# Kernel optimization log

Measured on AMD Instinct MI355X. Metric: run time of the kernel, lower is better.

The kernel has to match this reference:

```python
import jax, jax.numpy as jnp
import numpy as np

N = 50000      # nodes
E = 800000     # edges
NF = 128       # node_features
BF = 16        # bond_features
H = 4          # heads
C = 32         # hidden_size (per-head out channels)
HC = H * C     # 128 == NF, so all GAT layers share weight shape
DEPTH = 5
NEG_SLOPE = 0.2


def _sanitize(t):
    return jnp.nan_to_num(t, nan=0.0, posinf=1000.0, neginf=-1000.0)


def setup_inputs() -> dict:
    key = jax.random.key(0)
    ks = jax.random.split(key, 12)
    s = 0.1
    x = jax.random.normal(ks[0], (N, NF), jnp.float32)
    edge_index = jax.random.randint(ks[1], (2, E), 0, N, dtype=jnp.int32)
    edge_attr = jax.random.uniform(ks[2], (E, BF), jnp.float32)
    W = jax.random.normal(ks[3], (DEPTH, NF, HC), jnp.float32) * s
    att_src = jax.random.normal(ks[4], (DEPTH, H, C), jnp.float32) * s
    att_dst = jax.random.normal(ks[5], (DEPTH, H, C), jnp.float32) * s
    We = jax.random.normal(ks[6], (DEPTH, BF, HC), jnp.float32) * s
    att_edge = jax.random.normal(ks[7], (DEPTH, H, C), jnp.float32) * s
    b = jnp.zeros((DEPTH, HC), jnp.float32)
    Wout = jax.random.normal(ks[8], (NF + HC, C), jnp.float32) * s
    bout = jnp.zeros((C,), jnp.float32)
    return {"x": x, "edge_index": edge_index, "edge_attr": edge_attr,
            "W": W, "att_src": att_src, "att_dst": att_dst,
            "We": We, "att_edge": att_edge, "b": b,
            "Wout": Wout, "bout": bout}


def _gat_layer(h, s2, d2, ea, W_l, as_l, ad_l, We_l, ae_l, b_l):
    # h: [N, in_dim]; s2/d2: [E+N] edges incl. self loops; ea: [E+N, BF]
    xp = (h @ W_l).reshape(N, H, C)                     # lin(x), view per-head
    a_s = jnp.sum(xp * as_l, axis=-1)                   # [N, H]
    a_d = jnp.sum(xp * ad_l, axis=-1)                   # [N, H]
    ee = (ea @ We_l).reshape(-1, H, C)                  # lin_edge(edge_attr)
    a_e = jnp.sum(ee * ae_l, axis=-1)                   # [E+N, H]
    alpha = jax.nn.leaky_relu(a_s[s2] + a_d[d2] + a_e, NEG_SLOPE)
    # segment softmax over edges grouped by destination node
    m = jax.ops.segment_max(alpha, d2, num_segments=N)  # every node has a self loop -> finite
    ex = jnp.exp(alpha - m[d2])
    den = jax.ops.segment_sum(ex, d2, num_segments=N)
    coef = ex / (den[d2] + 1e-16)                       # [E+N, H]
    out = jax.ops.segment_sum(coef[:, :, None] * xp[s2], d2, num_segments=N)
    return out.reshape(N, HC) + b_l


def reference(x, edge_index, edge_attr, W, att_src, att_dst, We, att_edge, b, Wout, bout):
    src, dst = edge_index[0], edge_index[1]
    # add self loops with fill_value='mean': self-loop attr = mean of incoming edge_attr
    deg = jax.ops.segment_sum(jnp.ones((E,), edge_attr.dtype), dst, num_segments=N)
    sl_attr = jax.ops.segment_sum(edge_attr, dst, num_segments=N) / jnp.maximum(deg, 1.0)[:, None]
    ea = jnp.concatenate([edge_attr, sl_attr], axis=0)          # [E+N, BF]
    loop = jnp.arange(N, dtype=src.dtype)
    s2 = jnp.concatenate([src, loop])
    d2 = jnp.concatenate([dst, loop])

    h = _sanitize(x)
    for l in range(DEPTH):
        h = _gat_layer(h, s2, d2, ea, W[l], att_src[l], att_dst[l], We[l], att_edge[l], b[l])
        h = jax.nn.relu(h)            # dropout is a no-op in eval mode
        h = _sanitize(h)
    h_cat = jnp.concatenate([x, h], axis=1)             # [N, NF+HC]
    out = jax.nn.relu(h_cat @ Wout + bout)
    return _sanitize(out)
```

## Files before the change

kernel.cpp:

```cpp
#include <hip/hip_runtime.h>

#define NN 50000
#define NE 800000
#define NF 128
#define BF 16
#define NH 4
#define HC 128
#define CC 32
#define DEPTH 5
#define NEG 0.2f

typedef __attribute__((ext_vector_type(8))) short bf16x8;
typedef __attribute__((ext_vector_type(4))) float f32x4;

__device__ inline unsigned short f2bf(float f) {
  union { float f; unsigned u; } v; v.f = f;
  unsigned r = v.u + 0x7fff + ((v.u >> 16) & 1);
  return (unsigned short)(r >> 16);
}
__device__ inline float bf2f(unsigned short u) {
  union { unsigned u; float f; } v; v.u = (unsigned)u << 16; return v.f;
}

__global__ void k_count(const int* __restrict__ dst, int* __restrict__ deg) {
  int e = blockIdx.x * 256 + threadIdx.x;
  if (e < NE) atomicAdd(&deg[dst[e]], 1);
}

__global__ void k_partial(const int* __restrict__ deg, int* __restrict__ bsum) {
  __shared__ int s[256];
  int t = threadIdx.x;
  int i = blockIdx.x * 256 + t;
  s[t] = (i < NN) ? deg[i] : 0;
  __syncthreads();
  for (int d = 128; d > 0; d >>= 1) {
    if (t < d) s[t] += s[t + d];
    __syncthreads();
  }
  if (t == 0) bsum[blockIdx.x] = s[0];
}

__global__ void k_scan_top(int* __restrict__ bsum, int nb) {
  if (threadIdx.x == 0 && blockIdx.x == 0) {
    int run = 0;
    for (int i = 0; i < nb; ++i) { int v = bsum[i]; bsum[i] = run; run += v; }
  }
}

__global__ void k_scan_write(const int* __restrict__ deg, const int* __restrict__ bsum,
                             int* __restrict__ offs) {
  __shared__ int s[256];
  int t = threadIdx.x;
  int i = blockIdx.x * 256 + t;
  int v = (i < NN) ? deg[i] : 0;
  s[t] = v;
  __syncthreads();
  for (int d = 1; d < 256; d <<= 1) {
    int x = (t >= d) ? s[t - d] : 0;
    __syncthreads();
    s[t] += x;
    __syncthreads();
  }
  if (i < NN) offs[i] = bsum[blockIdx.x] + s[t] - v;
  if (i == 0) offs[NN] = NE;
}

__global__ void k_initcur(const int* __restrict__ offs, int* __restrict__ cur) {
  int i = blockIdx.x * 256 + threadIdx.x;
  if (i < NN) cur[i] = offs[i];
}

__global__ void k_fill(const int* __restrict__ src, const int* __restrict__ dst,
                       int* __restrict__ cur, int2* __restrict__ csr2) {
  int e = blockIdx.x * 256 + threadIdx.x;
  if (e < NE) {
    int slot = atomicAdd(&cur[dst[e]], 1);
    csr2[slot] = make_int2(e, src[e]);
  }
}

__global__ void k_weff(const float* __restrict__ We, const float* __restrict__ ae,
                       float* __restrict__ weff) {
  int idx = threadIdx.x;
  if (idx >= DEPTH * BF * NH) return;
  int l = idx / (BF * NH);
  int r = idx - l * (BF * NH);
  int f = r >> 2, h = r & 3;
  const float* We_l = We + (size_t)l * BF * HC;
  const float* ae_l = ae + (size_t)l * NH * CC;
  float acc = 0.f;
  for (int c = 0; c < CC; ++c) acc += We_l[f * HC + h * CC + c] * ae_l[h * CC + c];
  weff[idx] = acc;
}

__global__ __launch_bounds__(256) void k_aeprep(const int2* __restrict__ csr2,
                                                const float* __restrict__ eattr,
                                                const float* __restrict__ weff,
                                                unsigned short* __restrict__ ae_csr,
                                                int* __restrict__ csr_src) {
  __shared__ float sw[DEPTH * BF * NH];
  int t = threadIdx.x;
  if (t < DEPTH * BF * NH) sw[t] = weff[t];
  __syncthreads();
  int i = blockIdx.x * 256 + t;
  if (i >= NE) return;
  int2 c2 = csr2[i];
  int eid = c2.x;
  csr_src[i] = c2.y;
  float at[16];
  const float4* ar = (const float4*)(eattr + (size_t)eid * BF);
#pragma unroll
  for (int q = 0; q < 4; ++q) {
    float4 v = ar[q];
    at[q * 4] = v.x; at[q * 4 + 1] = v.y; at[q * 4 + 2] = v.z; at[q * 4 + 3] = v.w;
  }
#pragma unroll
  for (int l = 0; l < DEPTH; ++l) {
    float a0 = 0.f, a1 = 0.f, a2 = 0.f, a3 = 0.f;
#pragma unroll
    for (int f = 0; f < BF; ++f) {
      float av = at[f];
      const float* wf = &sw[(l * BF + f) * NH];
      a0 += av * wf[0]; a1 += av * wf[1]; a2 += av * wf[2]; a3 += av * wf[3];
    }
    ushort4 u;
    u.x = f2bf(a0); u.y = f2bf(a1); u.z = f2bf(a2); u.w = f2bf(a3);
    ((ushort4*)ae_csr)[(size_t)l * NE + i] = u;
  }
}

__global__ void k_aeself(const unsigned short* __restrict__ ae_csr,
                         const int* __restrict__ offs,
                         unsigned short* __restrict__ ae_self) {
  int idx = blockIdx.x * 256 + threadIdx.x;
  if (idx >= NN * DEPTH) return;
  int l = idx / NN, n = idx - l * NN;
  int s = offs[n], e = offs[n + 1];
  const ushort4* base = (const ushort4*)ae_csr + (size_t)l * NE;
  float a0 = 0.f, a1 = 0.f, a2 = 0.f, a3 = 0.f;
  for (int i = s; i < e; ++i) {
    ushort4 u = base[i];
    a0 += bf2f(u.x); a1 += bf2f(u.y); a2 += bf2f(u.z); a3 += bf2f(u.w);
  }
  float inv = 1.0f / fmaxf((float)(e - s), 1.0f);
  ushort4 o;
  o.x = f2bf(a0 * inv); o.y = f2bf(a1 * inv); o.z = f2bf(a2 * inv); o.w = f2bf(a3 * inv);
  ((ushort4*)ae_self)[(size_t)l * NN + n] = o;
}

__global__ void k_x2bf(const float* __restrict__ x, unsigned short* __restrict__ xb) {
  int i = blockIdx.x * 256 + threadIdx.x;
  if (i >= NN * 32) return;
  float4 v = ((const float4*)x)[i];
  ushort4 u;
  u.x = f2bf(v.x); u.y = f2bf(v.y); u.z = f2bf(v.z); u.w = f2bf(v.w);
  ((ushort4*)xb)[i] = u;
}

__global__ void k_wprep(const float* __restrict__ W, unsigned short* __restrict__ Wt) {
  int idx = blockIdx.x * 256 + threadIdx.x;
  if (idx >= DEPTH * NF * HC) return;
  int l = idx >> 14;
  int rem = idx & 16383;
  int n = rem >> 7, k = rem & 127;
  Wt[(size_t)l * 16384 + (size_t)n * 128 + k] = f2bf(W[(size_t)l * 16384 + (size_t)k * 128 + n]);
}

__global__ __launch_bounds__(256) void k_gemm_mfma(const unsigned short* __restrict__ Ab,
                                                   const unsigned short* __restrict__ Wt,
                                                   const float* __restrict__ as_w,
                                                   const float* __restrict__ ad_w,
                                                   unsigned short* __restrict__ xpb,
                                                   float* __restrict__ a_s,
                                                   float* __restrict__ a_d) {
  __shared__ unsigned short cl[64][144];
  __shared__ float swS[128], dwS[128];
  int t = threadIdx.x;
  if (t < 128) { swS[t] = as_w[t]; dwS[t] = ad_w[t]; }
  int wv = t >> 6;
  int l = t & 63;
  int r0 = blockIdx.x * 64;
  int lk = (l >> 4) * 8;
  int c0 = wv * 32;
  f32x4 acc[4][2] = {};
#pragma unroll
  for (int ks = 0; ks < 4; ++ks) {
    int kb = ks * 32 + lk;
    bf16x8 bfr0 = *(const bf16x8*)&Wt[(size_t)(c0 + (l & 15)) * 128 + kb];
    bf16x8 bfr1 = *(const bf16x8*)&Wt[(size_t)(c0 + 16 + (l & 15)) * 128 + kb];
#pragma unroll
    for (int rt = 0; rt < 4; ++rt) {
      int row = r0 + rt * 16 + (l & 15);
      row = row < NN ? row : NN - 1;
      bf16x8 afr = *(const bf16x8*)&Ab[(size_t)row * 128 + kb];
      acc[rt][0] = __builtin_amdgcn_mfma_f32_16x16x32_bf16(afr, bfr0, acc[rt][0], 0, 0, 0);
      acc[rt][1] = __builtin_amdgcn_mfma_f32_16x16x32_bf16(afr, bfr1, acc[rt][1], 0, 0, 0);
    }
  }
#pragma unroll
  for (int rt = 0; rt < 4; ++rt) {
#pragma unroll
    for (int j = 0; j < 4; ++j) {
      int lr = rt * 16 + (l >> 4) * 4 + j;
      cl[lr][c0 + (l & 15)] = f2bf(acc[rt][0][j]);
      cl[lr][c0 + 16 + (l & 15)] = f2bf(acc[rt][1][j]);
    }
  }
  __syncthreads();
  int row = t >> 2;
  int grow = r0 + row;
  int p = t & 3;
  if (grow < NN) {
    uint4* dst = (uint4*)&xpb[(size_t)grow * 128];
#pragma unroll
    for (int q = 0; q < 4; ++q)
      dst[q * 4 + p] = *(uint4*)&cl[row][(q * 4 + p) * 8];
  }
  int hh = t & 3;
  int hc = hh * 32;
  float ps = 0.f, pd = 0.f;
#pragma unroll
  for (int q = 0; q < 4; ++q) {
    uint4 u = *(uint4*)&cl[row][hc + q * 8];
    const unsigned short* us = (const unsigned short*)&u;
#pragma unroll
    for (int k = 0; k < 8; ++k) {
      float xv = bf2f(us[k]);
      ps += xv * swS[hc + q * 8 + k];
      pd += xv * dwS[hc + q * 8 + k];
    }
  }
  if (grow < NN) {
    a_s[(size_t)grow * 4 + hh] = ps;
    a_d[(size_t)grow * 4 + hh] = pd;
  }
}

__global__ __launch_bounds__(256) void k_aggr(const unsigned short* __restrict__ xpb,
                                              const unsigned short* __restrict__ ae_l,
                                              const unsigned short* __restrict__ aeself_l,
                                              const float* __restrict__ a_s,
                                              const float* __restrict__ a_d,
                                              const int* __restrict__ csr_src,
                                              const int* __restrict__ offs,
                                              const float* __restrict__ b_l,
                                              unsigned short* __restrict__ hout) {
  int node = blockIdx.x * 4 + (threadIdx.x >> 6);
  if (node >= NN) return;
  int lane = threadIdx.x & 63;
  int q = lane & 15;
  int h = lane >> 4;
  int base = lane & 48;
  const ushort2* xp2 = (const ushort2*)xpb;
  int s = offs[node], e = offs[node + 1];
  float ad = a_d[(size_t)node * 4 + h];
  float vs = a_s[(size_t)node * 4 + h] + ad + bf2f(aeself_l[(size_t)node * 4 + h]);
  vs = vs > 0.f ? vs : NEG * vs;
  float es = __expf(fminf(vs, 60.f));
  ushort2 xs = xp2[(size_t)node * 64 + lane];
  float acc0 = es * bf2f(xs.x), acc1 = es * bf2f(xs.y);
  float den = es;
  for (int i = s; i < e; i += 16) {
    int cnt = e - i;
    int srcv = 0;
    float w = 0.f;
    if (q < cnt) {
      srcv = csr_src[i + q];
      float a = a_s[(size_t)srcv * 4 + h] + ad + bf2f(ae_l[(size_t)(i + q) * 4 + h]);
      a = a > 0.f ? a : NEG * a;
      w = __expf(fminf(a, 60.f));
    }
#pragma unroll 8
    for (int qq = 0; qq < 16; ++qq) {
      int sq = __shfl(srcv, base | qq);
      float wq = __shfl(w, base | qq);
      ushort2 xq = xp2[(size_t)sq * 64 + lane];
      den += wq;
      acc0 += wq * bf2f(xq.x);
      acc1 += wq * bf2f(xq.y);
    }
  }
  float2 b2 = ((const float2*)b_l)[lane];
  float inv = 1.0f / (den + 1e-16f);
  float o0 = fmaxf(acc0 * inv + b2.x, 0.f);
  float o1 = fmaxf(acc1 * inv + b2.y, 0.f);
  ushort2 ho;
  ho.x = f2bf(o0); ho.y = f2bf(o1);
  ((ushort2*)hout)[(size_t)node * 64 + lane] = ho;
}

__global__ __launch_bounds__(256) void k_final(const float* __restrict__ x,
                                               const unsigned short* __restrict__ h,
                                               const float* __restrict__ Wout, const float* __restrict__ bout,
                                               float* __restrict__ out) {
  __shared__ float4 wlds[2048];
  int t = threadIdx.x;
#pragma unroll
  for (int i = 0; i < 8; ++i) wlds[t + i * 256] = ((const float4*)Wout)[t + i * 256];
  __syncthreads();
  int tx = t & 7;
  int ty = t >> 3;
  int row0 = blockIdx.x * 64 + ty;
  int row1 = row0 + 32;
  bool v0 = row0 < NN, v1 = row1 < NN;
  const float4* x4 = (const float4*)x;
  const ushort4* h4 = (const ushort4*)h;
  float acc[2][4] = {};
  const float4 z = make_float4(0.f, 0.f, 0.f, 0.f);
#pragma unroll 4
  for (int k4 = 0; k4 < 32; ++k4) {
    float4 a0 = v0 ? x4[(size_t)row0 * 32 + k4] : z;
    float4 a1 = v1 ? x4[(size_t)row1 * 32 + k4] : z;
    float av0[4] = {a0.x, a0.y, a0.z, a0.w};
    float av1[4] = {a1.x, a1.y, a1.z, a1.w};
#pragma unroll
    for (int kk = 0; kk < 4; ++kk) {
      float4 w = wlds[(k4 * 4 + kk) * 8 + tx];
      acc[0][0] += av0[kk] * w.x; acc[0][1] += av0[kk] * w.y;
      acc[0][2] += av0[kk] * w.z; acc[0][3] += av0[kk] * w.w;
      acc[1][0] += av1[kk] * w.x; acc[1][1] += av1[kk] * w.y;
      acc[1][2] += av1[kk] * w.z; acc[1][3] += av1[kk] * w.w;
    }
  }
#pragma unroll 4
  for (int k4 = 0; k4 < 32; ++k4) {
    ushort4 u0 = v0 ? h4[(size_t)row0 * 32 + k4] : make_ushort4(0, 0, 0, 0);
    ushort4 u1 = v1 ? h4[(size_t)row1 * 32 + k4] : make_ushort4(0, 0, 0, 0);
    float av0[4] = {bf2f(u0.x), bf2f(u0.y), bf2f(u0.z), bf2f(u0.w)};
    float av1[4] = {bf2f(u1.x), bf2f(u1.y), bf2f(u1.z), bf2f(u1.w)};
#pragma unroll
    for (int kk = 0; kk < 4; ++kk) {
      float4 w = wlds[(128 + k4 * 4 + kk) * 8 + tx];
      acc[0][0] += av0[kk] * w.x; acc[0][1] += av0[kk] * w.y;
      acc[0][2] += av0[kk] * w.z; acc[0][3] += av0[kk] * w.w;
      acc[1][0] += av1[kk] * w.x; acc[1][1] += av1[kk] * w.y;
      acc[1][2] += av1[kk] * w.z; acc[1][3] += av1[kk] * w.w;
    }
  }
  float4 b4 = ((const float4*)bout)[tx];
  if (v0) {
    float4 o = make_float4(fmaxf(acc[0][0] + b4.x, 0.f), fmaxf(acc[0][1] + b4.y, 0.f),
                           fmaxf(acc[0][2] + b4.z, 0.f), fmaxf(acc[0][3] + b4.w, 0.f));
    ((float4*)out)[(size_t)row0 * 8 + tx] = o;
  }
  if (v1) {
    float4 o = make_float4(fmaxf(acc[1][0] + b4.x, 0.f), fmaxf(acc[1][1] + b4.y, 0.f),
                           fmaxf(acc[1][2] + b4.z, 0.f), fmaxf(acc[1][3] + b4.w, 0.f));
    ((float4*)out)[(size_t)row1 * 8 + tx] = o;
  }
}

extern "C" void kernel_launch(void* const* d_in, const int* in_sizes, int n_in,
                              void* d_out, int out_size, void* d_ws, size_t ws_size,
                              hipStream_t stream) {
  const float* x        = (const float*)d_in[0];
  const int*   eidx     = (const int*)d_in[1];
  const float* eattr    = (const float*)d_in[2];
  const float* W        = (const float*)d_in[3];
  const float* att_src  = (const float*)d_in[4];
  const float* att_dst  = (const float*)d_in[5];
  const float* We       = (const float*)d_in[6];
  const float* att_edge = (const float*)d_in[7];
  const float* b        = (const float*)d_in[8];
  const float* Wout     = (const float*)d_in[9];
  const float* bout     = (const float*)d_in[10];
  float* out = (float*)d_out;

  const int* esrc = eidx;
  const int* edst = eidx + NE;

  size_t off = 0;
  auto carve = [&](size_t bytes) {
    void* p = (char*)d_ws + off;
    off += (bytes + 255) & ~(size_t)255;
    return p;
  };
  unsigned short* h_buf   = (unsigned short*)carve((size_t)NN * HC * 2);
  unsigned short* xpb     = (unsigned short*)carve((size_t)NN * HC * 2);
  unsigned short* Wt      = (unsigned short*)carve((size_t)DEPTH * NF * HC * 2);
  unsigned short* ae_csr  = (unsigned short*)carve((size_t)DEPTH * NE * NH * 2);
  unsigned short* ae_self = (unsigned short*)carve((size_t)DEPTH * NN * NH * 2);
  float* a_s   = (float*)carve((size_t)NN * NH * 4);
  float* a_d   = (float*)carve((size_t)NN * NH * 4);
  float* weff  = (float*)carve((size_t)DEPTH * BF * NH * 4);
  int* deg  = (int*)carve((size_t)NN * 4);
  int* offs = (int*)carve((size_t)(NN + 1) * 4);
  int* cur  = (int*)carve((size_t)NN * 4);
  int2* csr2 = (int2*)carve((size_t)NE * 8);
  int* csr_src = (int*)carve((size_t)NE * 4);
  int* bsum = (int*)carve(1024);

  const int nbN = (NN + 255) / 256;
  const int nbE = (NE + 255) / 256;

  hipMemsetAsync(deg, 0, (size_t)NN * 4, stream);
  k_count<<<nbE, 256, 0, stream>>>(edst, deg);
  k_partial<<<nbN, 256, 0, stream>>>(deg, bsum);
  k_scan_top<<<1, 64, 0, stream>>>(bsum, nbN);
  k_scan_write<<<nbN, 256, 0, stream>>>(deg, bsum, offs);
  k_initcur<<<nbN, 256, 0, stream>>>(offs, cur);
  k_fill<<<nbE, 256, 0, stream>>>(esrc, edst, cur, csr2);
  k_weff<<<1, 320, 0, stream>>>(We, att_edge, weff);
  k_aeprep<<<nbE, 256, 0, stream>>>(csr2, eattr, weff, ae_csr, csr_src);
  k_aeself<<<(NN * DEPTH + 255) / 256, 256, 0, stream>>>(ae_csr, offs, ae_self);
  k_x2bf<<<(NN * 32 + 255) / 256, 256, 0, stream>>>(x, h_buf);
  k_wprep<<<(DEPTH * NF * HC + 255) / 256, 256, 0, stream>>>(W, Wt);

  for (int l = 0; l < DEPTH; ++l) {
    k_gemm_mfma<<<(NN + 63) / 64, 256, 0, stream>>>(h_buf, Wt + (size_t)l * NF * HC,
                                                    att_src + (size_t)l * NH * CC,
                                                    att_dst + (size_t)l * NH * CC,
                                                    xpb, a_s, a_d);
    k_aggr<<<(NN + 3) / 4, 256, 0, stream>>>(xpb,
                                             ae_csr + (size_t)l * NE * NH,
                                             ae_self + (size_t)l * NN * NH,
                                             a_s, a_d, csr_src, offs,
                                             b + (size_t)l * HC, h_buf);
  }
  k_final<<<(NN + 63) / 64, 256, 0, stream>>>(x, h_buf, Wout, bout, out);
}
```

Before: 483.7 us.

## Replace atomic CSR fill with two-pass partitioned bucket scatter by destination

The single-kernel CSR fill, which scattered every edge to a random slot through global atomics, is replaced by a partitioned radix-style scatter. Edges are first bucketed into 256 coarse partitions keyed on dst>>8, using shared-memory counters, a partition scan and a staging buffer. A per-partition pass then does the fine atomic placement, so the cur/csr writes stay within a localized region. The aim is better locality for the atomics and scattered writes, at the cost of three extra kernel launches and an extra staging pass. k_aeprep now gathers the source index from esrc instead of reading it from the packed pair.

Measured after the change: 484.0 us. Within noise of the previous version (+0.1%).

```diff
diff --git a/kernel.cpp b/kernel.cpp
--- a/kernel.cpp
+++ b/kernel.cpp
@@ -9,6 +9,8 @@
 #define CC 32
 #define DEPTH 5
 #define NEG 0.2f
+#define NPART 256
+#define PTILE 4096
 
 typedef __attribute__((ext_vector_type(8))) short bf16x8;
 typedef __attribute__((ext_vector_type(4))) float f32x4;
@@ -70,12 +72,83 @@
   if (i < NN) cur[i] = offs[i];
 }
 
-__global__ void k_fill(const int* __restrict__ src, const int* __restrict__ dst,
-                       int* __restrict__ cur, int2* __restrict__ csr2) {
-  int e = blockIdx.x * 256 + threadIdx.x;
-  if (e < NE) {
-    int slot = atomicAdd(&cur[dst[e]], 1);
-    csr2[slot] = make_int2(e, src[e]);
+__global__ __launch_bounds__(256) void k_p0(const int* __restrict__ edst, int* __restrict__ pcnt) {
+  __shared__ int lc[NPART];
+  int t = threadIdx.x;
+  lc[t] = 0;
+  __syncthreads();
+  int base = blockIdx.x * PTILE;
+#pragma unroll
+  for (int j = 0; j < PTILE / 256; ++j) {
+    int e = base + t + j * 256;
+    if (e < NE) atomicAdd(&lc[edst[e] >> 8], 1);
+  }
+  __syncthreads();
+  if (lc[t]) atomicAdd(&pcnt[t], lc[t]);
+}
+
+__global__ void k_pscan(const int* __restrict__ pcnt, int* __restrict__ pbase,
+                        int* __restrict__ pcur) {
+  __shared__ int s[NPART];
+  int t = threadIdx.x;
+  int v = pcnt[t];
+  s[t] = v;
+  __syncthreads();
+  for (int d = 1; d < NPART; d <<= 1) {
+    int x = (t >= d) ? s[t - d] : 0;
+    __syncthreads();
+    s[t] += x;
+    __syncthreads();
+  }
+  int ex = s[t] - v;
+  pbase[t] = ex;
+  pcur[t] = ex;
+  if (t == NPART - 1) pbase[NPART] = s[NPART - 1];
+}
+
+__global__ __launch_bounds__(256) void k_p1(const int* __restrict__ edst,
+                                            int* __restrict__ pcur,
+                                            int2* __restrict__ staging) {
+  __shared__ int lc[NPART];
+  __shared__ int lbase[NPART];
+  __shared__ int lrank[NPART];
+  int t = threadIdx.x;
+  lc[t] = 0;
+  __syncthreads();
+  int base = blockIdx.x * PTILE;
+  int myd[PTILE / 256];
+#pragma unroll
+  for (int j = 0; j < PTILE / 256; ++j) {
+    int e = base + t + j * 256;
+    int d = (e < NE) ? edst[e] : -1;
+    myd[j] = d;
+    if (d >= 0) atomicAdd(&lc[d >> 8], 1);
+  }
+  __syncthreads();
+  if (lc[t]) lbase[t] = atomicAdd(&pcur[t], lc[t]);
+  lrank[t] = 0;
+  __syncthreads();
+#pragma unroll
+  for (int j = 0; j < PTILE / 256; ++j) {
+    int d = myd[j];
+    if (d >= 0) {
+      int p = d >> 8;
+      int r = atomicAdd(&lrank[p], 1);
+      staging[lbase[p] + r] = make_int2(base + t + j * 256, d);
+    }
+  }
+}
+
+__global__ __launch_bounds__(256) void k_p2(const int2* __restrict__ staging,
+                                            const int* __restrict__ pbase,
+                                            int* __restrict__ cur,
+                                            int* __restrict__ csr_eid) {
+  int p = blockIdx.x;
+  int s = pbase[p], e = pbase[p + 1];
+  for (int i = s + threadIdx.x; i < e; i += 256) {
+    int2 st = staging[i];
+    int slot = atomicAdd(&cur[st.y], 1);
+    csr_eid[slot] = st.x;
   }
 }
 
@@ -93,7 +166,8 @@
   weff[idx] = acc;
 }
 
-__global__ __launch_bounds__(256) void k_aeprep(const int2* __restrict__ csr2,
+__global__ __launch_bounds__(256) void k_aeprep(const int* __restrict__ csr_eid,
+                                                const int* __restrict__ esrc,
                                                 const float* __restrict__ eattr,
                                                 const float* __restrict__ weff,
                                                 unsigned short* __restrict__ ae_csr,
@@ -104,9 +178,8 @@
   __syncthreads();
   int i = blockIdx.x * 256 + t;
   if (i >= NE) return;
-  int2 c2 = csr2[i];
-  int eid = c2.x;
-  csr_src[i] = c2.y;
+  int eid = csr_eid[i];
+  csr_src[i] = esrc[eid];
   float at[16];
   const float4* ar = (const float4*)(eattr + (size_t)eid * BF);
 #pragma unroll
@@ -386,22 +459,31 @@
   int* deg  = (int*)carve((size_t)NN * 4);
   int* offs = (int*)carve((size_t)(NN + 1) * 4);
   int* cur  = (int*)carve((size_t)NN * 4);
-  int2* csr2 = (int2*)carve((size_t)NE * 8);
+  int2* staging = (int2*)carve((size_t)NE * 8);
+  int* csr_eid = (int*)carve((size_t)NE * 4);
   int* csr_src = (int*)carve((size_t)NE * 4);
+  int* pcnt  = (int*)carve((size_t)NPART * 4);
+  int* pbase = (int*)carve((size_t)(NPART + 1) * 4);
+  int* pcur  = (int*)carve((size_t)NPART * 4);
   int* bsum = (int*)carve(1024);
 
   const int nbN = (NN + 255) / 256;
   const int nbE = (NE + 255) / 256;
+  const int nbP = (NE + PTILE - 1) / PTILE;
 
   hipMemsetAsync(deg, 0, (size_t)NN * 4, stream);
+  hipMemsetAsync(pcnt, 0, (size_t)NPART * 4, stream);
   k_count<<<nbE, 256, 0, stream>>>(edst, deg);
   k_partial<<<nbN, 256, 0, stream>>>(deg, bsum);
   k_scan_top<<<1, 64, 0, stream>>>(bsum, nbN);
   k_scan_write<<<nbN, 256, 0, stream>>>(deg, bsum, offs);
   k_initcur<<<nbN, 256, 0, stream>>>(offs, cur);
-  k_fill<<<nbE, 256, 0, stream>>>(esrc, edst, cur, csr2);
+  k_p0<<<nbP, 256, 0, stream>>>(edst, pcnt);
+  k_pscan<<<1, NPART, 0, stream>>>(pcnt, pbase, pcur);
+  k_p1<<<nbP, 256, 0, stream>>>(edst, pcur, staging);
+  k_p2<<<NPART, 256, 0, stream>>>(staging, pbase, cur, csr_eid);
   k_weff<<<1, 320, 0, stream>>>(We, att_edge, weff);
-  k_aeprep<<<nbE, 256, 0, stream>>>(csr2, eattr, weff, ae_csr, csr_src);
+  k_aeprep<<<nbE, 256, 0, stream>>>(csr_eid, esrc, eattr, weff, ae_csr, csr_src);
   k_aeself<<<(NN * DEPTH + 255) / 256, 256, 0, stream>>>(ae_csr, offs, ae_self);
   k_x2bf<<<(NN * 32 + 255) / 256, 256, 0, stream>>>(x, h_buf);
   k_wprep<<<(DEPTH * NF * HC + 255) / 256, 256, 0, stream>>>(W, Wt);
```
